# Kernel tuning notes

Measured on AMD Instinct MI355X. Metric: run time of the kernel, lower is better.

The kernel has to match this reference:

```python
import jax, jax.numpy as jnp
import numpy as np


def _unfold9(t):
    """F.unfold equivalent for [B,1,H,W], kernel 3x3, pad 1, stride 1 -> [B,9,H*W].
    Row order matches torch: k = ki*3 + kj over the 3x3 window."""
    B, C, H, W = t.shape
    p = jnp.pad(t, ((0, 0), (0, 0), (1, 1), (1, 1)))
    patches = jnp.stack([p[:, 0, i:i + H, j:j + W] for i in range(3) for j in range(3)], axis=1)
    return patches.reshape(B, 9, H * W)


def setup_inputs() -> dict:
    key = jax.random.key(0)
    ks = jax.random.split(key, 7)
    B, H, W, O = 8, 64, 1024, 32
    mk = lambda k: jax.random.normal(k, (B, 1, H, W), dtype=jnp.float32)
    x = mk(ks[0])
    X = mk(ks[1])
    A = mk(ks[2])
    E = mk(ks[3])
    # validity mask (float, mostly ones)
    M = (jax.random.uniform(ks[4], (B, 1, H, W)) > 0.1).astype(jnp.float32)
    conv_w = jax.random.normal(ks[5], (O, 4), dtype=jnp.float32) * 0.5  # Conv1d(4,O,1) weight squeezed
    conv_b = jax.random.normal(ks[6], (O,), dtype=jnp.float32) * 0.1
    return {"x": x, "X": X, "A": A, "E": E, "M": M, "conv_w": conv_w, "conv_b": conv_b}


def reference(x, X, A, E, M, conv_w, conv_b):
    B, _, H, W = x.shape
    L = H * W
    ux = _unfold9(x)   # [B,9,L]
    uX = _unfold9(X)
    uA = _unfold9(A)
    uE = _unfold9(E)
    uM = _unfold9(M)
    # center values, broadcast over the 9 neighbors (== repeat_interleave by 9)
    Xc = X.reshape(B, 1, L)
    Ac = A.reshape(B, 1, L)
    Ec = E.reshape(B, 1, L)
    Mc = M.reshape(B, 1, L)
    Ad = uA - Ac
    Ed = uE - Ec
    cA, sA = jnp.cos(Ad), jnp.sin(Ad)
    cE, sE = jnp.cos(Ed), jnp.sin(Ed)
    f1 = ux * cA * cE - Xc
    f2 = ux * cA * sE
    f3 = ux * sA
    feats = jnp.stack([ux, f1, f2, f3], axis=1)  # [B,4,9,L]
    # 1x1 Conv1d over channel dim 4 -> O
    out = jnp.einsum('bfkl,of->bokl', feats, conv_w) + conv_b[None, :, None, None]  # [B,O,9,L]
    Mv = (Mc * uM)[:, None, :, :]  # [B,1,9,L]
    out = out * Mv
    out = jnp.max(out, axis=2)  # masked max over 9 neighbors -> [B,O,L]
    return out.reshape(B, -1, H, W)
```

## Files before the change

### kernel.cpp

```cpp
#include <hip/hip_runtime.h>
#include <hip/hip_bf16.h>

#define NO 32
#define HH 64
#define WW 1024
#define LL (HH * WW)
#define BB 8
#define TW 258
#define TSZ 774

typedef _Float16 h2 __attribute__((ext_vector_type(2)));
typedef _Float16 v8h __attribute__((ext_vector_type(8)));
typedef float f32x16 __attribute__((ext_vector_type(16)));
typedef unsigned u32x4v __attribute__((ext_vector_type(4)));

static __device__ __forceinline__ unsigned pku(float a, float b) {
    return __builtin_bit_cast(unsigned, __builtin_amdgcn_cvt_pkrtz(a, b));
}
static __device__ __forceinline__ float lo16f(unsigned u) {
    return (float)__builtin_bit_cast(h2, u).x;
}
static __device__ __forceinline__ float hi16f(unsigned u) {
    return (float)__builtin_bit_cast(h2, u).y;
}

__global__ __launch_bounds__(256, 4) void pnc_kernel(
    const float* __restrict__ x, const float* __restrict__ X,
    const float* __restrict__ A, const float* __restrict__ E,
    const float* __restrict__ M, const float* __restrict__ cw,
    const float* __restrict__ cb, float* __restrict__ out)
{
    __shared__ unsigned tA[TSZ];
    __shared__ unsigned tE[TSZ];
    __shared__ unsigned tXM[TSZ];

    const int tid = threadIdx.x;
    const int bi  = blockIdx.x;
    const int b   = bi >> 8;
    const int h   = (bi >> 2) & 63;
    const int wq  = (bi & 3) << 8;
    const int w   = wq + tid;
    const int l   = (h << 10) + w;

    const float* xb = x + b * LL;
    const float* Xb = X + b * LL;
    const float* Ab = A + b * LL;
    const float* Eb = E + b * LL;
    const float* Mb = M + b * LL;

    float av[4], ev[4], xv[4], mv[4];
    #pragma unroll
    for (int i = 0; i < 4; ++i) {
        const int s = tid + (i << 8);
        const int r = (s >= 2 * TW) ? 2 : ((s >= TW) ? 1 : 0);
        const int c = s - r * TW;
        int gh = h - 1 + r;  gh = min(max(gh, 0), HH - 1);
        int gw = wq - 1 + c; gw = min(max(gw, 0), WW - 1);
        const int gl = (gh << 10) + gw;
        if (i < 3 || s < TSZ) {
            av[i] = Ab[gl]; ev[i] = Eb[gl];
            xv[i] = xb[gl]; mv[i] = Mb[gl];
        } else { av[i] = 0.f; ev[i] = 0.f; xv[i] = 0.f; mv[i] = 0.f; }
    }
    const float Xc = Xb[l];
    const int o_ln = tid & 31;
    const float4 wv = ((const float4*)cw)[o_ln];
    const float  bo = cb[o_ln];

    #pragma unroll
    for (int i = 0; i < 4; ++i) {
        const int s = tid + (i << 8);
        if (i == 3 && s >= TSZ) continue;
        float sa, ca, se, ce;
        __sincosf(av[i], &sa, &ca);
        __sincosf(ev[i], &se, &ce);
        tA[s]  = pku(sa, ca);
        tE[s]  = pku(se, ce);
        tXM[s] = pku(xv[i], mv[i]);
    }
    __syncthreads();

    const int cl = tid + 1;
    const unsigned cA_ = tA[TW + cl], cE_ = tE[TW + cl], cX_ = tXM[TW + cl];
    const float sAc = lo16f(cA_), cAc = hi16f(cA_);
    const float sEc = lo16f(cE_), cEc = hi16f(cE_);
    const float Mc  = hi16f(cX_);

    const unsigned a0 = pku(wv.x, wv.y);
    const unsigned a1 = pku(wv.z, wv.w);
    const unsigned a2 = pku(bo, 0.f);
    const bool lol = ((tid & 63) < 32);
    const v8h A1 = __builtin_bit_cast(v8h,
        (u32x4v){lol ? a0 : 0u, lol ? a1 : 0u, lol ? a2 : 0u, 0u});
    const v8h A2 = __builtin_bit_cast(v8h,
        (u32x4v){lol ? 0u : a0, lol ? 0u : a1, lol ? 0u : a2, 0u});

    f32x16 zz;
    #pragma unroll
    for (int i = 0; i < 16; ++i) zz[i] = 0.f;

    f32x16 R1, R2;
    #pragma unroll
    for (int k = 0; k < 9; ++k) {
        const int r  = k / 3;
        const int cc = k % 3;
        const int hh = h + r - 1, ww = w + cc - 1;
        const bool valid = ((unsigned)hh < (unsigned)HH) &
                           ((unsigned)ww < (unsigned)WW);
        const int ts = r * TW + tid + cc;
        const unsigned pa = tA[ts], pe = tE[ts], pxm = tXM[ts];
        const float ux = lo16f(pxm);
        const float um = hi16f(pxm);
        const float mm = valid ? (Mc * um) : 0.f;
        const float sAu = lo16f(pa), cAu = hi16f(pa);
        const float sEu = lo16f(pe), cEu = hi16f(pe);
        const float cA2 = __fmaf_rn(cAu, cAc, sAu * sAc);
        const float sA2 = __fmaf_rn(sAu, cAc, -(cAu * sAc));
        const float cE2 = __fmaf_rn(cEu, cEc, sEu * sEc);
        const float sE2 = __fmaf_rn(sEu, cEc, -(cEu * sEc));
        const float xcA = ux * cA2;
        const float f0 = ux;
        const float f1 = __fmaf_rn(xcA, cE2, -Xc);
        const float f2 = xcA * sE2;
        const float f3 = ux * sA2;
        const v8h Bk = __builtin_bit_cast(v8h,
            (u32x4v){pku(mm * f0, mm * f1), pku(mm * f2, mm * f3),
                     pku(mm, 0.f), 0u});
        const f32x16 D1 = __builtin_amdgcn_mfma_f32_32x32x16_f16(A1, Bk, zz, 0, 0, 0);
        const f32x16 D2 = __builtin_amdgcn_mfma_f32_32x32x16_f16(A2, Bk, zz, 0, 0, 0);
        if (k == 0) { R1 = D1; R2 = D2; }
        else {
            R1 = __builtin_elementwise_max(R1, D1);
            R2 = __builtin_elementwise_max(R2, D2);
        }
    }

    const int lane = tid & 63;
    const int wid  = tid >> 6;
    const int c31  = lane & 31;
    const int hi   = lane >> 5;
    float* ob0 = out + (b * NO + hi * 4) * LL + (h << 10) + wq + (wid << 6) + c31;
    #pragma unroll
    for (int i = 0; i < 16; ++i) {
        const int oo = (i & 3) + 8 * (i >> 2);
        __builtin_nontemporal_store(R1[i], ob0 + oo * LL);
        __builtin_nontemporal_store(R2[i], ob0 + oo * LL + 32);
    }
}

extern "C" void kernel_launch(void* const* d_in, const int* in_sizes, int n_in,
                              void* d_out, int out_size, void* d_ws, size_t ws_size,
                              hipStream_t stream) {
    const float* x  = (const float*)d_in[0];
    const float* X  = (const float*)d_in[1];
    const float* A  = (const float*)d_in[2];
    const float* E  = (const float*)d_in[3];
    const float* M  = (const float*)d_in[4];
    const float* cw = (const float*)d_in[5];
    const float* cb = (const float*)d_in[6];
    float* out = (float*)d_out;

    pnc_kernel<<<BB * 64 * 4, 256, 0, stream>>>(x, X, A, E, M, cw, cb, out);
}
```

Baseline: 18.79 us.

## Process two full rows per 1024-thread block to reuse halo tiles

Each block now covers two full image rows (1024 columns) using 1024 threads, staging four halo rows in LDS instead of three rows of a 256-column segment. This cuts redundant halo loads and sincos work, since vertical overlap drops from 3x to 2x and horizontal edge overlap disappears. In exchange there are only 256 blocks of 1024 threads, which may leave many CUs underused on a large GPU, and launch_bounds(1024,4) may pressure registers with two sets of outputs.

```diff
diff --git a/kernel.cpp b/kernel.cpp
--- a/kernel.cpp
+++ b/kernel.cpp
@@ -6,8 +6,8 @@
 #define WW 1024
 #define LL (HH * WW)
 #define BB 8
-#define TW 258
-#define TSZ 774
+#define TW 1026
+#define TSZ (4 * TW)
 
 typedef _Float16 h2 __attribute__((ext_vector_type(2)));
 typedef _Float16 v8h __attribute__((ext_vector_type(8)));
@@ -24,7 +24,7 @@
     return (float)__builtin_bit_cast(h2, u).y;
 }
 
-__global__ __launch_bounds__(256, 4) void pnc_kernel(
+__global__ __launch_bounds__(1024, 4) void pnc_kernel(
     const float* __restrict__ x, const float* __restrict__ X,
     const float* __restrict__ A, const float* __restrict__ E,
     const float* __restrict__ M, const float* __restrict__ cw,
@@ -36,11 +36,8 @@
 
     const int tid = threadIdx.x;
     const int bi  = blockIdx.x;
-    const int b   = bi >> 8;
-    const int h   = (bi >> 2) & 63;
-    const int wq  = (bi & 3) << 8;
-    const int w   = wq + tid;
-    const int l   = (h << 10) + w;
+    const int b   = bi >> 5;
+    const int h0  = (bi & 31) << 1;
 
     const float* xb = x + b * LL;
     const float* Xb = X + b * LL;
@@ -48,29 +45,28 @@
     const float* Eb = E + b * LL;
     const float* Mb = M + b * LL;
 
-    float av[4], ev[4], xv[4], mv[4];
+    float av[5], ev[5], xv[5], mv[5];
     #pragma unroll
-    for (int i = 0; i < 4; ++i) {
-        const int s = tid + (i << 8);
-        const int r = (s >= 2 * TW) ? 2 : ((s >= TW) ? 1 : 0);
+    for (int i = 0; i < 5; ++i) {
+        const int s = tid + (i << 10);
+        if (i == 4 && s >= TSZ) { av[i] = ev[i] = xv[i] = mv[i] = 0.f; continue; }
+        const int r = (s >= 3 * TW) ? 3 : ((s >= 2 * TW) ? 2 : ((s >= TW) ? 1 : 0));
         const int c = s - r * TW;
-        int gh = h - 1 + r;  gh = min(max(gh, 0), HH - 1);
-        int gw = wq - 1 + c; gw = min(max(gw, 0), WW - 1);
+        int gh = h0 - 1 + r; gh = min(max(gh, 0), HH - 1);
+        int gw = c - 1;      gw = min(max(gw, 0), WW - 1);
         const int gl = (gh << 10) + gw;
-        if (i < 3 || s < TSZ) {
-            av[i] = Ab[gl]; ev[i] = Eb[gl];
-            xv[i] = xb[gl]; mv[i] = Mb[gl];
-        } else { av[i] = 0.f; ev[i] = 0.f; xv[i] = 0.f; mv[i] = 0.f; }
+        av[i] = Ab[gl]; ev[i] = Eb[gl];
+        xv[i] = xb[gl]; mv[i] = Mb[gl];
     }
-    const float Xc = Xb[l];
+    const float Xcv[2] = { Xb[(h0 << 10) + tid], Xb[((h0 + 1) << 10) + tid] };
     const int o_ln = tid & 31;
     const float4 wv = ((const float4*)cw)[o_ln];
     const float  bo = cb[o_ln];
 
     #pragma unroll
-    for (int i = 0; i < 4; ++i) {
-        const int s = tid + (i << 8);
-        if (i == 3 && s >= TSZ) continue;
+    for (int i = 0; i < 5; ++i) {
+        const int s = tid + (i << 10);
+        if (i == 4 && s >= TSZ) continue;
         float sa, ca, se, ce;
         __sincosf(av[i], &sa, &ca);
         __sincosf(ev[i], &se, &ce);
@@ -79,12 +75,6 @@
         tXM[s] = pku(xv[i], mv[i]);
     }
     __syncthreads();
-
-    const int cl = tid + 1;
-    const unsigned cA_ = tA[TW + cl], cE_ = tE[TW + cl], cX_ = tXM[TW + cl];
-    const float sAc = lo16f(cA_), cAc = hi16f(cA_);
-    const float sEc = lo16f(cE_), cEc = hi16f(cE_);
-    const float Mc  = hi16f(cX_);
 
     const unsigned a0 = pku(wv.x, wv.y);
     const unsigned a1 = pku(wv.z, wv.w);
@@ -99,52 +89,64 @@
     #pragma unroll
     for (int i = 0; i < 16; ++i) zz[i] = 0.f;
 
-    f32x16 R1, R2;
-    #pragma unroll
-    for (int k = 0; k < 9; ++k) {
-        const int r  = k / 3;
-        const int cc = k % 3;
-        const int hh = h + r - 1, ww = w + cc - 1;
-        const bool valid = ((unsigned)hh < (unsigned)HH) &
-                           ((unsigned)ww < (unsigned)WW);
-        const int ts = r * TW + tid + cc;
-        const unsigned pa = tA[ts], pe = tE[ts], pxm = tXM[ts];
-        const float ux = lo16f(pxm);
-        const float um = hi16f(pxm);
-        const float mm = valid ? (Mc * um) : 0.f;
-        const float sAu = lo16f(pa), cAu = hi16f(pa);
-        const float sEu = lo16f(pe), cEu = hi16f(pe);
-        const float cA2 = __fmaf_rn(cAu, cAc, sAu * sAc);
-        const float sA2 = __fmaf_rn(sAu, cAc, -(cAu * sAc));
-        const float cE2 = __fmaf_rn(cEu, cEc, sEu * sEc);
-        const float sE2 = __fmaf_rn(sEu, cEc, -(cEu * sEc));
-        const float xcA = ux * cA2;
-        const float f0 = ux;
-        const float f1 = __fmaf_rn(xcA, cE2, -Xc);
-        const float f2 = xcA * sE2;
-        const float f3 = ux * sA2;
-        const v8h Bk = __builtin_bit_cast(v8h,
-            (u32x4v){pku(mm * f0, mm * f1), pku(mm * f2, mm * f3),
-                     pku(mm, 0.f), 0u});
-        const f32x16 D1 = __builtin_amdgcn_mfma_f32_32x32x16_f16(A1, Bk, zz, 0, 0, 0);
-        const f32x16 D2 = __builtin_amdgcn_mfma_f32_32x32x16_f16(A2, Bk, zz, 0, 0, 0);
-        if (k == 0) { R1 = D1; R2 = D2; }
-        else {
-            R1 = __builtin_elementwise_max(R1, D1);
-            R2 = __builtin_elementwise_max(R2, D2);
-        }
-    }
-
     const int lane = tid & 63;
     const int wid  = tid >> 6;
     const int c31  = lane & 31;
     const int hi   = lane >> 5;
-    float* ob0 = out + (b * NO + hi * 4) * LL + (h << 10) + wq + (wid << 6) + c31;
+
     #pragma unroll
-    for (int i = 0; i < 16; ++i) {
-        const int oo = (i & 3) + 8 * (i >> 2);
-        __builtin_nontemporal_store(R1[i], ob0 + oo * LL);
-        __builtin_nontemporal_store(R2[i], ob0 + oo * LL + 32);
+    for (int set = 0; set < 2; ++set) {
+        const int hrow = h0 + set;
+        const int ctr  = (set + 1) * TW + tid + 1;
+        const unsigned cA_ = tA[ctr], cE_ = tE[ctr], cX_ = tXM[ctr];
+        const float sAc = lo16f(cA_), cAc = hi16f(cA_);
+        const float sEc = lo16f(cE_), cEc = hi16f(cE_);
+        const float Mc  = hi16f(cX_);
+        const float Xc  = Xcv[set];
+
+        f32x16 R1, R2;
+        #pragma unroll
+        for (int k = 0; k < 9; ++k) {
+            const int r  = k / 3;
+            const int cc = k % 3;
+            const int hh = hrow + r - 1, ww = tid + cc - 1;
+            const bool valid = ((unsigned)hh < (unsigned)HH) &
+                               ((unsigned)ww < (unsigned)WW);
+            const int ts = (set + r) * TW + tid + cc;
+            const unsigned pa = tA[ts], pe = tE[ts], pxm = tXM[ts];
+            const float ux = lo16f(pxm);
+            const float um = hi16f(pxm);
+            const float mm = valid ? (Mc * um) : 0.f;
+            const float sAu = lo16f(pa), cAu = hi16f(pa);
+            const float sEu = lo16f(pe), cEu = hi16f(pe);
+            const float cA2 = __fmaf_rn(cAu, cAc, sAu * sAc);
+            const float sA2 = __fmaf_rn(sAu, cAc, -(cAu * sAc));
+            const float cE2 = __fmaf_rn(cEu, cEc, sEu * sEc);
+            const float sE2 = __fmaf_rn(sEu, cEc, -(cEu * sEc));
+            const float xcA = ux * cA2;
+            const float f0 = ux;
+            const float f1 = __fmaf_rn(xcA, cE2, -Xc);
+            const float f2 = xcA * sE2;
+            const float f3 = ux * sA2;
+            const v8h Bk = __builtin_bit_cast(v8h,
+                (u32x4v){pku(mm * f0, mm * f1), pku(mm * f2, mm * f3),
+                         pku(mm, 0.f), 0u});
+            const f32x16 D1 = __builtin_amdgcn_mfma_f32_32x32x16_f16(A1, Bk, zz, 0, 0, 0);
+            const f32x16 D2 = __builtin_amdgcn_mfma_f32_32x32x16_f16(A2, Bk, zz, 0, 0, 0);
+            if (k == 0) { R1 = D1; R2 = D2; }
+            else {
+                R1 = __builtin_elementwise_max(R1, D1);
+                R2 = __builtin_elementwise_max(R2, D2);
+            }
+        }
+
+        float* ob0 = out + (b * NO + hi * 4) * LL + (hrow << 10) + (wid << 6) + c31;
+        #pragma unroll
+        for (int i = 0; i < 16; ++i) {
+            const int oo = (i & 3) + 8 * (i >> 2);
+            __builtin_nontemporal_store(R1[i], ob0 + oo * LL);
+            __builtin_nontemporal_store(R2[i], ob0 + oo * LL + 32);
+        }
     }
 }
 
@@ -160,5 +162,5 @@
     const float* cb = (const float*)d_in[6];
     float* out = (float*)d_out;
 
-    pnc_kernel<<<BB * 64 * 4, 256, 0, stream>>>(x, X, A, E, M, cw, cb, out);
+    pnc_kernel<<<BB * 32, 1024, 0, stream>>>(x, X, A, E, M, cw, cb, out);
 }
```

Result: slower. 45.33 us (+141.3%).
